# Kernel tuning notes

Hardware: AMD Instinct MI355X
Metric: run time of the kernel (lower is better)

## Reference

```python
import jax, jax.numpy as jnp
import numpy as np

EXP, MAN = 8, 23  # exponent/mantissa bits of the simulated float format


def float_quantize(x, exp=EXP, man=MAN):
    """Round-to-nearest-even quantization to a float format with `exp` exponent
    bits and `man` mantissa bits (faithful to mptorch float_quantize 'nearest').
    With exp=8, man=23 this is an exact identity on fp32 inputs."""
    emax = 2 ** (exp - 1) - 1          # max unbiased exponent
    emin = 1 - emax                     # min normal exponent (clamping here yields subnormal grid)
    ax = jnp.abs(x)
    e = jnp.clip(jnp.floor(jnp.log2(jnp.where(ax > 0, ax, 1.0))), emin, emax)
    # scale mantissa into [1,2), round to `man` fractional bits (ties-to-even via jnp.round)
    m = jnp.round(x * jnp.exp2(-e) * (2.0 ** man)) * (2.0 ** -man)
    q = m * jnp.exp2(e)
    maxval = (2.0 - 2.0 ** -man) * (2.0 ** emax)
    q = jnp.clip(q, -maxval, maxval)
    return jnp.where(ax == 0, x, q).astype(x.dtype)


def setup_inputs() -> dict:
    key = jax.random.key(0)
    k1, k2, k3 = jax.random.split(key, 3)
    M, IN, OUT = 8192, 1024, 4096
    x = jax.random.normal(k1, (M, IN), dtype=jnp.float32)
    # kaiming-uniform-ish scale for weight, 1/sqrt(fan_in) for bias
    bound_w = float(np.sqrt(1.0 / IN))
    weight = jax.random.uniform(k2, (OUT, IN), dtype=jnp.float32, minval=-bound_w, maxval=bound_w)
    bias = jax.random.uniform(k3, (OUT,), dtype=jnp.float32, minval=-bound_w, maxval=bound_w)
    return {"x": x, "weight": weight, "bias": bias}


def reference(x, weight, bias):
    # QLinearFunction.forward: quantize weight, quant_gemm, add quantized bias, quantize output.
    # quant_gemm with (man=23, exp=8) simulates fp32 multiply-accumulate, i.e. a plain
    # fp32 GEMM; we express it as matmul followed by output quantization.
    qweight = float_quantize(weight)                 # [OUT, IN]
    out = jnp.matmul(x, qweight.T)                   # [M, OUT], fp32 accumulate
    out = out + float_quantize(bias)[None, :]
    return float_quantize(out)
```

## Files before the change

kernel.cpp:

```cpp
#include <hip/hip_runtime.h>
#include <stdint.h>

#define MM 8192
#define KK 1024
#define NN 4096

#define BM 128
#define BN 128
#define BK 64

using f32x4 = __attribute__((ext_vector_type(4))) float;
using u16x8 = __attribute__((ext_vector_type(8))) unsigned short;

static __device__ __forceinline__ unsigned short f2bf(float f) {
    unsigned int u = __builtin_bit_cast(unsigned int, f);
    u += 0x7fffu + ((u >> 16) & 1u);
    return (unsigned short)(u >> 16);
}
static __device__ __forceinline__ float bf2f(unsigned short s) {
    unsigned int u = ((unsigned int)s) << 16;
    return __builtin_bit_cast(float, u);
}

__global__ __launch_bounds__(256) void split_hi_lo(const float* __restrict__ in,
                                                   unsigned short* __restrict__ hi,
                                                   unsigned short* __restrict__ lo,
                                                   int n8) {
    int i = blockIdx.x * 256 + threadIdx.x;
    if (i >= n8) return;
    const float4* p = (const float4*)in + (size_t)i * 2;
    float4 a = p[0], b = p[1];
    float v[8] = {a.x, a.y, a.z, a.w, b.x, b.y, b.z, b.w};
    u16x8 h, l;
#pragma unroll
    for (int j = 0; j < 8; ++j) {
        unsigned short hb = f2bf(v[j]);
        h[j] = hb;
        l[j] = f2bf(v[j] - bf2f(hb));
    }
    *((u16x8*)hi + i) = h;
    *((u16x8*)lo + i) = l;
}

static __device__ __forceinline__ void mfma16(f32x4& d, u16x8 a, u16x8 b) {
    asm("v_mfma_f32_16x16x32_bf16 %0, %1, %2, %0" : "+v"(d) : "v"(a), "v"(b));
}

__global__ __launch_bounds__(256, 2) void qlinear_mfma(
        const unsigned short* __restrict__ Ah, const unsigned short* __restrict__ Al,
        const unsigned short* __restrict__ Bh, const unsigned short* __restrict__ Bl,
        const float* __restrict__ bias, float* __restrict__ out) {
    __shared__ __attribute__((aligned(16))) unsigned short sAh[BM * BK];
    __shared__ __attribute__((aligned(16))) unsigned short sAl[BM * BK];
    __shared__ __attribute__((aligned(16))) unsigned short sBh[BN * BK];
    __shared__ __attribute__((aligned(16))) unsigned short sBl[BN * BK];

    int bid = blockIdx.x;
    int wg = (bid & 7) * 256 + (bid >> 3);
    int bm = wg & 63;
    int bn = wg >> 6;

    const int t = threadIdx.x;
    const int lane = t & 63;
    const int wid = t >> 6;

    const int wr = (wid >> 1) * 64;
    const int wc = (wid & 1) * 64;
    const int lr = lane & 15;
    const int lg = lane >> 4;

    f32x4 acc[4][4] = {};

    for (int kt = 0; kt < KK; kt += BK) {
        __syncthreads();
#pragma unroll
        for (int i = 0; i < 4; ++i) {
            int o = i * 256 + t;
            int row = o >> 3;
            int k0 = (o & 7) * 8;
            int sidx = row * BK + (k0 ^ ((row & 7) << 3));
            size_t ga = (size_t)(bm * BM + row) * KK + kt + k0;
            size_t gb = (size_t)(bn * BN + row) * KK + kt + k0;
            *(u16x8*)(sAh + sidx) = *(const u16x8*)(Ah + ga);
            *(u16x8*)(sAl + sidx) = *(const u16x8*)(Al + ga);
            *(u16x8*)(sBh + sidx) = *(const u16x8*)(Bh + gb);
            *(u16x8*)(sBl + sidx) = *(const u16x8*)(Bl + gb);
        }
        __syncthreads();

#pragma unroll
        for (int kk = 0; kk < 2; ++kk) {
            const int kb = kk * 32 + lg * 8;
            u16x8 ah[4], al[4], bh[4], bl[4];
#pragma unroll
            for (int mi = 0; mi < 4; ++mi) {
                int row = wr + mi * 16 + lr;
                int idx = row * BK + (kb ^ ((row & 7) << 3));
                ah[mi] = *(const u16x8*)(sAh + idx);
                al[mi] = *(const u16x8*)(sAl + idx);
            }
#pragma unroll
            for (int ni = 0; ni < 4; ++ni) {
                int row = wc + ni * 16 + lr;
                int idx = row * BK + (kb ^ ((row & 7) << 3));
                bh[ni] = *(const u16x8*)(sBh + idx);
                bl[ni] = *(const u16x8*)(sBl + idx);
            }
#pragma unroll
            for (int mi = 0; mi < 4; ++mi) {
#pragma unroll
                for (int ni = 0; ni < 4; ++ni) {
                    mfma16(acc[mi][ni], ah[mi], bh[ni]);
                    mfma16(acc[mi][ni], al[mi], bh[ni]);
                    mfma16(acc[mi][ni], ah[mi], bl[ni]);
                }
            }
        }
    }

    const int colbase = bn * BN + wc;
    const int rowbase = bm * BM + wr;
    float bv[4];
#pragma unroll
    for (int ni = 0; ni < 4; ++ni) bv[ni] = bias[colbase + ni * 16 + lr];
#pragma unroll
    for (int mi = 0; mi < 4; ++mi) {
#pragma unroll
        for (int ni = 0; ni < 4; ++ni) {
            int col = colbase + ni * 16 + lr;
            size_t base = (size_t)(rowbase + mi * 16 + lg * 4) * NN + col;
#pragma unroll
            for (int r = 0; r < 4; ++r)
                out[base + (size_t)r * NN] = acc[mi][ni][r] + bv[ni];
        }
    }
}

__global__ __launch_bounds__(256) void qlinear_naive(const float* __restrict__ x,
                                                     const float* __restrict__ w,
                                                     const float* __restrict__ bias,
                                                     float* __restrict__ out) {
    int n = blockIdx.x * 64 + (threadIdx.x & 63);
    int m = blockIdx.y * 4 + (threadIdx.x >> 6);
    const float4* xr = (const float4*)(x + (size_t)m * KK);
    const float4* wr = (const float4*)(w + (size_t)n * KK);
    float s = 0.f;
    for (int k = 0; k < KK / 4; ++k) {
        float4 a = xr[k], b = wr[k];
        s += a.x * b.x + a.y * b.y + a.z * b.z + a.w * b.w;
    }
    out[(size_t)m * NN + n] = s + bias[n];
}

extern "C" void kernel_launch(void* const* d_in, const int* in_sizes, int n_in,
                              void* d_out, int out_size, void* d_ws, size_t ws_size,
                              hipStream_t stream) {
    (void)in_sizes; (void)n_in; (void)out_size;
    const float* x = (const float*)d_in[0];
    const float* w = (const float*)d_in[1];
    const float* bias = (const float*)d_in[2];
    float* out = (float*)d_out;

    const size_t xcnt = (size_t)MM * KK;
    const size_t wcnt = (size_t)NN * KK;
    const size_t need = (xcnt + wcnt) * 2 * sizeof(unsigned short);

    if (ws_size >= need) {
        unsigned short* xh = (unsigned short*)d_ws;
        unsigned short* xl = xh + xcnt;
        unsigned short* wh = xl + xcnt;
        unsigned short* wl = wh + wcnt;
        split_hi_lo<<<(int)(xcnt / 8 / 256), 256, 0, stream>>>(x, xh, xl, (int)(xcnt / 8));
        split_hi_lo<<<(int)(wcnt / 8 / 256), 256, 0, stream>>>(w, wh, wl, (int)(wcnt / 8));
        qlinear_mfma<<<2048, 256, 0, stream>>>(xh, xl, wh, wl, bias, out);
    } else {
        dim3 grid(NN / 64, MM / 4);
        qlinear_naive<<<grid, 256, 0, stream>>>(x, w, bias, out);
    }
}
```

Measured before the change: 347.8 us.

## Pre-pack tiles and double-buffer 256x256 MFMA GEMM with direct global-to-LDS loads

The split kernel now writes the bf16 hi/lo operands in a pre-tiled, pre-swizzled layout, so every K-tile is one contiguous block. The GEMM switches to 256x256 tiles with 512 threads and a double-buffered LDS. It fills the next buffer with global_load_lds while MFMAs run, interleaving LDS reads, barriers and priority hints in phases. The goal is to hide global-load latency and raise per-block data reuse, at the cost of larger register and LDS use and fewer blocks (512).

```diff
diff --git a/kernel.cpp b/kernel.cpp
--- a/kernel.cpp
+++ b/kernel.cpp
@@ -4,13 +4,13 @@
 #define MM 8192
 #define KK 1024
 #define NN 4096
-
-#define BM 128
-#define BN 128
-#define BK 64
-
-using f32x4 = __attribute__((ext_vector_type(4))) float;
-using u16x8 = __attribute__((ext_vector_type(8))) unsigned short;
+#define NT 32
+#define TE 8192
+#define PL 16384
+
+typedef float f32x4 __attribute__((ext_vector_type(4)));
+typedef __bf16 bf16x8 __attribute__((ext_vector_type(8)));
+typedef unsigned short u16x8 __attribute__((ext_vector_type(8)));
 
 static __device__ __forceinline__ unsigned short f2bf(float f) {
     unsigned int u = __builtin_bit_cast(unsigned int, f);
@@ -22,14 +22,16 @@
     return __builtin_bit_cast(float, u);
 }
 
-__global__ __launch_bounds__(256) void split_hi_lo(const float* __restrict__ in,
-                                                   unsigned short* __restrict__ hi,
-                                                   unsigned short* __restrict__ lo,
-                                                   int n8) {
+__global__ __launch_bounds__(256) void split_pack(const float* __restrict__ in,
+        unsigned short* __restrict__ hi, unsigned short* __restrict__ lo, int total) {
     int i = blockIdx.x * 256 + threadIdx.x;
-    if (i >= n8) return;
-    const float4* p = (const float4*)in + (size_t)i * 2;
-    float4 a = p[0], b = p[1];
+    if (i >= total) return;
+    int row = i >> 7;
+    int og  = i & 127;
+    int kt  = og >> 2, oct = og & 3;
+    int bt  = row >> 8, r = row & 255;
+    const float4* s = (const float4*)(in + (size_t)row * KK + kt * 32 + oct * 8);
+    float4 a = s[0], b = s[1];
     float v[8] = {a.x, a.y, a.z, a.w, b.x, b.y, b.z, b.w};
     u16x8 h, l;
 #pragma unroll
@@ -38,102 +40,150 @@
         h[j] = hb;
         l[j] = f2bf(v[j] - bf2f(hb));
     }
-    *((u16x8*)hi + i) = h;
-    *((u16x8*)lo + i) = l;
-}
-
-static __device__ __forceinline__ void mfma16(f32x4& d, u16x8 a, u16x8 b) {
-    asm("v_mfma_f32_16x16x32_bf16 %0, %1, %2, %0" : "+v"(d) : "v"(a), "v"(b));
-}
-
-__global__ __launch_bounds__(256, 2) void qlinear_mfma(
+    int slot = r * 4 + (oct ^ ((r >> 1) & 3));
+    size_t off = (size_t)(bt * NT + kt) * TE + (size_t)slot * 8;
+    *(u16x8*)(hi + off) = h;
+    *(u16x8*)(lo + off) = l;
+}
+
+static __device__ __forceinline__ bf16x8 ldsr(unsigned addr) {
+    bf16x8 r;
+    asm volatile("ds_read_b128 %0, %1" : "=v"(r) : "v"(addr));
+    return r;
+}
+static __device__ __forceinline__ void gl16(const unsigned short* g, unsigned short* l) {
+    __builtin_amdgcn_global_load_lds(
+        (__attribute__((address_space(1))) void*)(void*)g,
+        (__attribute__((address_space(3))) void*)(void*)l, 16, 0, 0);
+}
+static __device__ __forceinline__ void mf(f32x4& d, bf16x8 a, bf16x8 b) {
+    d = __builtin_amdgcn_mfma_f32_16x16x32_bf16(a, b, d, 0, 0, 0);
+}
+
+#define PHASE_PRE() \
+    __builtin_amdgcn_s_barrier(); \
+    asm volatile("s_waitcnt lgkmcnt(0)" ::: "memory"); \
+    __builtin_amdgcn_sched_barrier(0); \
+    __builtin_amdgcn_s_setprio(1);
+#define PHASE_POST() \
+    __builtin_amdgcn_s_setprio(0); \
+    __builtin_amdgcn_s_barrier();
+#define CLUSTER(M0, M1) \
+    _Pragma("unroll") \
+    for (int ni = 0; ni < 4; ++ni) { \
+        mf(acc[M0][ni], a0, bh[ni]); mf(acc[M0][ni], l0, bh[ni]); mf(acc[M0][ni], a0, blo[ni]); \
+        mf(acc[M1][ni], a1, bh[ni]); mf(acc[M1][ni], l1, bh[ni]); mf(acc[M1][ni], a1, blo[ni]); \
+    }
+
+__global__ __launch_bounds__(512, 2) void qlinear_mfma(
         const unsigned short* __restrict__ Ah, const unsigned short* __restrict__ Al,
         const unsigned short* __restrict__ Bh, const unsigned short* __restrict__ Bl,
         const float* __restrict__ bias, float* __restrict__ out) {
-    __shared__ __attribute__((aligned(16))) unsigned short sAh[BM * BK];
-    __shared__ __attribute__((aligned(16))) unsigned short sAl[BM * BK];
-    __shared__ __attribute__((aligned(16))) unsigned short sBh[BN * BK];
-    __shared__ __attribute__((aligned(16))) unsigned short sBl[BN * BK];
+    __shared__ __attribute__((aligned(16))) unsigned short S[2][4][TE];
 
     int bid = blockIdx.x;
-    int wg = (bid & 7) * 256 + (bid >> 3);
-    int bm = wg & 63;
-    int bn = wg >> 6;
-
-    const int t = threadIdx.x;
-    const int lane = t & 63;
-    const int wid = t >> 6;
-
-    const int wr = (wid >> 1) * 64;
-    const int wc = (wid & 1) * 64;
-    const int lr = lane & 15;
-    const int lg = lane >> 4;
-
-    f32x4 acc[4][4] = {};
-
-    for (int kt = 0; kt < KK; kt += BK) {
-        __syncthreads();
-#pragma unroll
-        for (int i = 0; i < 4; ++i) {
-            int o = i * 256 + t;
-            int row = o >> 3;
-            int k0 = (o & 7) * 8;
-            int sidx = row * BK + (k0 ^ ((row & 7) << 3));
-            size_t ga = (size_t)(bm * BM + row) * KK + kt + k0;
-            size_t gb = (size_t)(bn * BN + row) * KK + kt + k0;
-            *(u16x8*)(sAh + sidx) = *(const u16x8*)(Ah + ga);
-            *(u16x8*)(sAl + sidx) = *(const u16x8*)(Al + ga);
-            *(u16x8*)(sBh + sidx) = *(const u16x8*)(Bh + gb);
-            *(u16x8*)(sBl + sidx) = *(const u16x8*)(Bl + gb);
-        }
-        __syncthreads();
-
-#pragma unroll
-        for (int kk = 0; kk < 2; ++kk) {
-            const int kb = kk * 32 + lg * 8;
-            u16x8 ah[4], al[4], bh[4], bl[4];
-#pragma unroll
-            for (int mi = 0; mi < 4; ++mi) {
-                int row = wr + mi * 16 + lr;
-                int idx = row * BK + (kb ^ ((row & 7) << 3));
-                ah[mi] = *(const u16x8*)(sAh + idx);
-                al[mi] = *(const u16x8*)(sAl + idx);
-            }
-#pragma unroll
-            for (int ni = 0; ni < 4; ++ni) {
-                int row = wc + ni * 16 + lr;
-                int idx = row * BK + (kb ^ ((row & 7) << 3));
-                bh[ni] = *(const u16x8*)(sBh + idx);
-                bl[ni] = *(const u16x8*)(sBl + idx);
-            }
-#pragma unroll
-            for (int mi = 0; mi < 4; ++mi) {
-#pragma unroll
-                for (int ni = 0; ni < 4; ++ni) {
-                    mfma16(acc[mi][ni], ah[mi], bh[ni]);
-                    mfma16(acc[mi][ni], al[mi], bh[ni]);
-                    mfma16(acc[mi][ni], ah[mi], bl[ni]);
-                }
-            }
-        }
-    }
-
-    const int colbase = bn * BN + wc;
-    const int rowbase = bm * BM + wr;
+    int wg = (bid & 7) * 64 + (bid >> 3);
+    int bm = wg & 31, bn = wg >> 5;
+
+    const int tix = threadIdx.x;
+    const int lane = tix & 63, wid = tix >> 6;
+    const int wr = (wid >> 2) * 128, wc = (wid & 3) * 64;
+    const int lr = lane & 15, lg = lane >> 4;
+    const int xorv = (lr >> 1) & 3;
+
+    const unsigned lb = (unsigned)(uintptr_t)(__attribute__((address_space(3))) void*)&S[0][0][0];
+    const unsigned pA = lb + (unsigned)(((wr + lr) * 32 + (lg ^ xorv) * 8) * 2);
+    const unsigned pB = lb + (unsigned)(((wc + lr) * 32 + (lg ^ xorv) * 8) * 2);
+
+    const int soff = wid * 1024 + lane * 8;
+    const unsigned short* sAh = Ah + (size_t)bm * NT * TE + soff;
+    const unsigned short* sAl = Al + (size_t)bm * NT * TE + soff;
+    const unsigned short* sBh = Bh + (size_t)bn * NT * TE + soff;
+    const unsigned short* sBl = Bl + (size_t)bn * NT * TE + soff;
+
+    f32x4 acc[8][4];
+#pragma unroll
+    for (int mi = 0; mi < 8; ++mi)
+#pragma unroll
+        for (int ni = 0; ni < 4; ++ni) acc[mi][ni] = (f32x4){0.f, 0.f, 0.f, 0.f};
+
+    gl16(sAh,       &S[0][0][wid * 1024]);
+    gl16(sAh + 512, &S[0][0][wid * 1024 + 512]);
+    gl16(sAl,       &S[0][1][wid * 1024]);
+    gl16(sAl + 512, &S[0][1][wid * 1024 + 512]);
+    gl16(sBh,       &S[0][2][wid * 1024]);
+    gl16(sBh + 512, &S[0][2][wid * 1024 + 512]);
+    gl16(sBl,       &S[0][3][wid * 1024]);
+    gl16(sBl + 512, &S[0][3][wid * 1024 + 512]);
+    asm volatile("s_waitcnt vmcnt(0)" ::: "memory");
+    __builtin_amdgcn_s_barrier();
+
+    for (int t = 0; t < NT; ++t) {
+        const unsigned bo = (unsigned)(t & 1) * (4 * PL);
+        const int nb = (t & 1) ^ 1;
+        const size_t st = (size_t)(t + 1) * TE;
+        const bool pf = (t + 1 < NT);
+
+        bf16x8 bh[4], blo[4], a0, a1, l0, l1;
+
+#pragma unroll
+        for (int ni = 0; ni < 4; ++ni) {
+            bh[ni]  = ldsr(pB + bo + 2 * PL + ni * 1024);
+            blo[ni] = ldsr(pB + bo + 3 * PL + ni * 1024);
+        }
+        a0 = ldsr(pA + bo);        l0 = ldsr(pA + bo + PL);
+        a1 = ldsr(pA + bo + 1024); l1 = ldsr(pA + bo + PL + 1024);
+        if (pf) {
+            gl16(sAh + st,       &S[nb][0][wid * 1024]);
+            gl16(sAh + st + 512, &S[nb][0][wid * 1024 + 512]);
+            gl16(sAl + st,       &S[nb][1][wid * 1024]);
+            gl16(sAl + st + 512, &S[nb][1][wid * 1024 + 512]);
+        }
+        PHASE_PRE();
+        CLUSTER(0, 1);
+        PHASE_POST();
+
+        a0 = ldsr(pA + bo + 2 * 1024); l0 = ldsr(pA + bo + PL + 2 * 1024);
+        a1 = ldsr(pA + bo + 3 * 1024); l1 = ldsr(pA + bo + PL + 3 * 1024);
+        if (pf) {
+            gl16(sBh + st,       &S[nb][2][wid * 1024]);
+            gl16(sBh + st + 512, &S[nb][2][wid * 1024 + 512]);
+            gl16(sBl + st,       &S[nb][3][wid * 1024]);
+            gl16(sBl + st + 512, &S[nb][3][wid * 1024 + 512]);
+        }
+        PHASE_PRE();
+        CLUSTER(2, 3);
+        PHASE_POST();
+
+        a0 = ldsr(pA + bo + 4 * 1024); l0 = ldsr(pA + bo + PL + 4 * 1024);
+        a1 = ldsr(pA + bo + 5 * 1024); l1 = ldsr(pA + bo + PL + 5 * 1024);
+        PHASE_PRE();
+        CLUSTER(4, 5);
+        PHASE_POST();
+
+        a0 = ldsr(pA + bo + 6 * 1024); l0 = ldsr(pA + bo + PL + 6 * 1024);
+        a1 = ldsr(pA + bo + 7 * 1024); l1 = ldsr(pA + bo + PL + 7 * 1024);
+        PHASE_PRE();
+        CLUSTER(6, 7);
+        __builtin_amdgcn_s_setprio(0);
+        asm volatile("s_waitcnt vmcnt(0)" ::: "memory");
+        __builtin_amdgcn_s_barrier();
+    }
+
+    const int row0 = bm * 256 + wr + lg * 4;
+    const int col0 = bn * 256 + wc + lr;
     float bv[4];
 #pragma unroll
-    for (int ni = 0; ni < 4; ++ni) bv[ni] = bias[colbase + ni * 16 + lr];
-#pragma unroll
-    for (int mi = 0; mi < 4; ++mi) {
+    for (int ni = 0; ni < 4; ++ni) bv[ni] = bias[col0 + ni * 16];
+#pragma unroll
+    for (int mi = 0; mi < 8; ++mi)
 #pragma unroll
         for (int ni = 0; ni < 4; ++ni) {
-            int col = colbase + ni * 16 + lr;
-            size_t base = (size_t)(rowbase + mi * 16 + lg * 4) * NN + col;
+            float* o = out + (size_t)(row0 + mi * 16) * NN + col0 + ni * 16;
 #pragma unroll
             for (int r = 0; r < 4; ++r)
-                out[base + (size_t)r * NN] = acc[mi][ni][r] + bv[ni];
-        }
-    }
+                o[(size_t)r * NN] = acc[mi][ni][r] + bv[ni];
+        }
 }
 
 __global__ __launch_bounds__(256) void qlinear_naive(const float* __restrict__ x,
@@ -170,9 +220,9 @@
         unsigned short* xl = xh + xcnt;
         unsigned short* wh = xl + xcnt;
         unsigned short* wl = wh + wcnt;
-        split_hi_lo<<<(int)(xcnt / 8 / 256), 256, 0, stream>>>(x, xh, xl, (int)(xcnt / 8));
-        split_hi_lo<<<(int)(wcnt / 8 / 256), 256, 0, stream>>>(w, wh, wl, (int)(wcnt / 8));
-        qlinear_mfma<<<2048, 256, 0, stream>>>(xh, xl, wh, wl, bias, out);
+        split_pack<<<(int)(MM * 128 / 256), 256, 0, stream>>>(x, xh, xl, MM * 128);
+        split_pack<<<(int)(NN * 128 / 256), 256, 0, stream>>>(w, wh, wl, NN * 128);
+        qlinear_mfma<<<512, 512, 0, stream>>>(xh, xl, wh, wl, bias, out);
     } else {
         dim3 grid(NN / 64, MM / 4);
         qlinear_naive<<<grid, 256, 0, stream>>>(x, w, bias, out);
```

Measured after the change: 335.3 us. -3.6%, faster.

## Pre-pack operands into MFMA fragment layout and use 32x32 MFMA with direct register A loads

Applied to the files above, without the earlier changes.

The split kernels now write bf16 hi/lo data in a tile-major fragment order. The A operand is loaded straight from global memory into registers, and the B operand is streamed into double-buffered LDS with global_load_lds. The GEMM changes to 256x128 tiles using 32x32x16 bf16 MFMA, with software prefetch of the next k-step and setprio around MFMA blocks. The aim is to remove LDS staging and bank traffic for A, cut LDS read instructions, and overlap loads with compute. In exchange it uses more registers, and A reuse across warps relies on L2/cache rather than shared memory.

```diff
diff --git a/kernel.cpp b/kernel.cpp
--- a/kernel.cpp
+++ b/kernel.cpp
@@ -4,13 +4,11 @@
 #define MM 8192
 #define KK 1024
 #define NN 4096
-
-#define BM 128
-#define BN 128
-#define BK 64
-
-using f32x4 = __attribute__((ext_vector_type(4))) float;
-using u16x8 = __attribute__((ext_vector_type(8))) unsigned short;
+#define NT 32
+
+typedef float f32x16 __attribute__((ext_vector_type(16)));
+typedef __bf16 bf16x8 __attribute__((ext_vector_type(8)));
+typedef unsigned short u16x8 __attribute__((ext_vector_type(8)));
 
 static __device__ __forceinline__ unsigned short f2bf(float f) {
     unsigned int u = __builtin_bit_cast(unsigned int, f);
@@ -22,14 +20,14 @@
     return __builtin_bit_cast(float, u);
 }
 
-__global__ __launch_bounds__(256) void split_hi_lo(const float* __restrict__ in,
-                                                   unsigned short* __restrict__ hi,
-                                                   unsigned short* __restrict__ lo,
-                                                   int n8) {
+__global__ __launch_bounds__(256) void pack_a(const float* __restrict__ x,
+        unsigned short* __restrict__ Ah, unsigned short* __restrict__ Al) {
     int i = blockIdx.x * 256 + threadIdx.x;
-    if (i >= n8) return;
-    const float4* p = (const float4*)in + (size_t)i * 2;
-    float4 a = p[0], b = p[1];
+    int lane = i & 63, fb = (i >> 6) & 15, kt = (i >> 10) & 31, bm = i >> 15;
+    int row = bm * 256 + (fb >> 1) * 32 + (lane & 31);
+    int k   = kt * 32 + (fb & 1) * 16 + (lane >> 5) * 8;
+    const float4* s = (const float4*)(x + (size_t)row * KK + k);
+    float4 a = s[0], b = s[1];
     float v[8] = {a.x, a.y, a.z, a.w, b.x, b.y, b.z, b.w};
     u16x8 h, l;
 #pragma unroll
@@ -38,102 +36,153 @@
         h[j] = hb;
         l[j] = f2bf(v[j] - bf2f(hb));
     }
-    *((u16x8*)hi + i) = h;
-    *((u16x8*)lo + i) = l;
-}
-
-static __device__ __forceinline__ void mfma16(f32x4& d, u16x8 a, u16x8 b) {
-    asm("v_mfma_f32_16x16x32_bf16 %0, %1, %2, %0" : "+v"(d) : "v"(a), "v"(b));
+    *(u16x8*)(Ah + (size_t)i * 8) = h;
+    *(u16x8*)(Al + (size_t)i * 8) = l;
+}
+
+__global__ __launch_bounds__(256) void pack_b(const float* __restrict__ w,
+        unsigned short* __restrict__ Bpk) {
+    int i = blockIdx.x * 256 + threadIdx.x;
+    int lane = i & 63, fb = (i >> 6) & 7, kt = (i >> 9) & 31, bn = i >> 14;
+    int col = bn * 128 + (fb >> 1) * 32 + (lane & 31);
+    int k   = kt * 32 + (fb & 1) * 16 + (lane >> 5) * 8;
+    const float4* s = (const float4*)(w + (size_t)col * KK + k);
+    float4 a = s[0], b = s[1];
+    float v[8] = {a.x, a.y, a.z, a.w, b.x, b.y, b.z, b.w};
+    u16x8 h, l;
+#pragma unroll
+    for (int j = 0; j < 8; ++j) {
+        unsigned short hb = f2bf(v[j]);
+        h[j] = hb;
+        l[j] = f2bf(v[j] - bf2f(hb));
+    }
+    size_t tb = ((size_t)bn * 32 + kt) * 8192;
+    *(u16x8*)(Bpk + tb + fb * 512 + lane * 8) = h;
+    *(u16x8*)(Bpk + tb + 4096 + fb * 512 + lane * 8) = l;
+}
+
+static __device__ __forceinline__ void gl16(const unsigned short* g, unsigned short* l) {
+    __builtin_amdgcn_global_load_lds(
+        (__attribute__((address_space(1))) void*)(void*)g,
+        (__attribute__((address_space(3))) void*)(void*)l, 16, 0, 0);
+}
+static __device__ __forceinline__ void mf(f32x16& d, bf16x8 a, bf16x8 b) {
+    d = __builtin_amdgcn_mfma_f32_32x32x16_bf16(a, b, d, 0, 0, 0);
 }
 
 __global__ __launch_bounds__(256, 2) void qlinear_mfma(
         const unsigned short* __restrict__ Ah, const unsigned short* __restrict__ Al,
-        const unsigned short* __restrict__ Bh, const unsigned short* __restrict__ Bl,
+        const unsigned short* __restrict__ Bpk,
         const float* __restrict__ bias, float* __restrict__ out) {
-    __shared__ __attribute__((aligned(16))) unsigned short sAh[BM * BK];
-    __shared__ __attribute__((aligned(16))) unsigned short sAl[BM * BK];
-    __shared__ __attribute__((aligned(16))) unsigned short sBh[BN * BK];
-    __shared__ __attribute__((aligned(16))) unsigned short sBl[BN * BK];
+    __shared__ __attribute__((aligned(16))) unsigned short sB[2 * 8192];
 
     int bid = blockIdx.x;
-    int wg = (bid & 7) * 256 + (bid >> 3);
-    int bm = wg & 63;
-    int bn = wg >> 6;
-
-    const int t = threadIdx.x;
-    const int lane = t & 63;
-    const int wid = t >> 6;
-
-    const int wr = (wid >> 1) * 64;
-    const int wc = (wid & 1) * 64;
-    const int lr = lane & 15;
-    const int lg = lane >> 4;
-
-    f32x4 acc[4][4] = {};
-
-    for (int kt = 0; kt < KK; kt += BK) {
+    int xc = bid & 7, s = bid >> 3;
+    int bm = (xc & 3) * 8 + (s & 7);
+    int bn = (xc >> 2) * 16 + (s >> 3);
+
+    const int tid = threadIdx.x;
+    const int lane = tid & 63, wid = tid >> 6;
+    const int wrb = (wid >> 1) * 4;
+    const int wcb = (wid & 1) * 2;
+
+    const size_t aoff = (size_t)bm * 262144 + (size_t)wrb * 1024 + lane * 8;
+    const size_t bsrc = (size_t)bn * 262144 + tid * 8;
+    const unsigned boff = wcb * 1024 + lane * 8;
+
+    f32x16 acc[4][2];
+#pragma unroll
+    for (int mi = 0; mi < 4; ++mi)
+#pragma unroll
+        for (int ni = 0; ni < 2; ++ni)
+#pragma unroll
+            for (int r = 0; r < 16; ++r) acc[mi][ni][r] = 0.f;
+
+    bf16x8 A0h[4], A0l[4], A1h[4], A1l[4];
+
+#define LDA(H, L, T, KS) do { _Pragma("unroll") \
+    for (int mi = 0; mi < 4; ++mi) { \
+        H[mi] = *(const bf16x8*)(Ah + aoff + (size_t)(T) * 8192 + mi * 1024 + (KS) * 512); \
+        L[mi] = *(const bf16x8*)(Al + aoff + (size_t)(T) * 8192 + mi * 1024 + (KS) * 512); \
+    } } while (0)
+#define STB(T, NB) do { _Pragma("unroll") \
+    for (int j = 0; j < 4; ++j) \
+        gl16(Bpk + bsrc + (size_t)(T) * 8192 + j * 2048, \
+             sB + (NB) * 8192 + j * 2048 + tid * 8); } while (0)
+
+    LDA(A0h, A0l, 0, 0);
+    LDA(A1h, A1l, 0, 1);
+    STB(0, 0);
+    __syncthreads();
+
+    for (int t = 0; t < NT; ++t) {
+        const int cur = t & 1, nb = cur ^ 1;
+        const unsigned short* sb = sB + cur * 8192;
+
+        bf16x8 B0h[2], B0l[2], B1h[2], B1l[2];
+#pragma unroll
+        for (int ni = 0; ni < 2; ++ni) {
+            B0h[ni] = *(const bf16x8*)(sb + boff + ni * 1024);
+            B0l[ni] = *(const bf16x8*)(sb + 4096 + boff + ni * 1024);
+        }
+        if (t + 1 < NT) STB(t + 1, nb);
+
+        __builtin_amdgcn_s_setprio(1);
+#pragma unroll
+        for (int mi = 0; mi < 4; ++mi)
+#pragma unroll
+            for (int ni = 0; ni < 2; ++ni) mf(acc[mi][ni], A0h[mi], B0h[ni]);
+#pragma unroll
+        for (int mi = 0; mi < 4; ++mi)
+#pragma unroll
+            for (int ni = 0; ni < 2; ++ni) mf(acc[mi][ni], A0l[mi], B0h[ni]);
+#pragma unroll
+        for (int mi = 0; mi < 4; ++mi)
+#pragma unroll
+            for (int ni = 0; ni < 2; ++ni) mf(acc[mi][ni], A0h[mi], B0l[ni]);
+        __builtin_amdgcn_s_setprio(0);
+        __builtin_amdgcn_sched_barrier(0);
+        if (t + 1 < NT) LDA(A0h, A0l, t + 1, 0);
+
+#pragma unroll
+        for (int ni = 0; ni < 2; ++ni) {
+            B1h[ni] = *(const bf16x8*)(sb + boff + ni * 1024 + 512);
+            B1l[ni] = *(const bf16x8*)(sb + 4096 + boff + ni * 1024 + 512);
+        }
+        __builtin_amdgcn_s_setprio(1);
+#pragma unroll
+        for (int mi = 0; mi < 4; ++mi)
+#pragma unroll
+            for (int ni = 0; ni < 2; ++ni) mf(acc[mi][ni], A1h[mi], B1h[ni]);
+#pragma unroll
+        for (int mi = 0; mi < 4; ++mi)
+#pragma unroll
+            for (int ni = 0; ni < 2; ++ni) mf(acc[mi][ni], A1l[mi], B1h[ni]);
+#pragma unroll
+        for (int mi = 0; mi < 4; ++mi)
+#pragma unroll
+            for (int ni = 0; ni < 2; ++ni) mf(acc[mi][ni], A1h[mi], B1l[ni]);
+        __builtin_amdgcn_s_setprio(0);
+        __builtin_amdgcn_sched_barrier(0);
+        if (t + 1 < NT) LDA(A1h, A1l, t + 1, 1);
+
         __syncthreads();
-#pragma unroll
-        for (int i = 0; i < 4; ++i) {
-            int o = i * 256 + t;
-            int row = o >> 3;
-            int k0 = (o & 7) * 8;
-            int sidx = row * BK + (k0 ^ ((row & 7) << 3));
-            size_t ga = (size_t)(bm * BM + row) * KK + kt + k0;
-            size_t gb = (size_t)(bn * BN + row) * KK + kt + k0;
-            *(u16x8*)(sAh + sidx) = *(const u16x8*)(Ah + ga);
-            *(u16x8*)(sAl + sidx) = *(const u16x8*)(Al + ga);
-            *(u16x8*)(sBh + sidx) = *(const u16x8*)(Bh + gb);
-            *(u16x8*)(sBl + sidx) = *(const u16x8*)(Bl + gb);
-        }
-        __syncthreads();
-
-#pragma unroll
-        for (int kk = 0; kk < 2; ++kk) {
-            const int kb = kk * 32 + lg * 8;
-            u16x8 ah[4], al[4], bh[4], bl[4];
-#pragma unroll
-            for (int mi = 0; mi < 4; ++mi) {
-                int row = wr + mi * 16 + lr;
-                int idx = row * BK + (kb ^ ((row & 7) << 3));
-                ah[mi] = *(const u16x8*)(sAh + idx);
-                al[mi] = *(const u16x8*)(sAl + idx);
+    }
+#undef LDA
+#undef STB
+
+    const int row0 = bm * 256 + (wid >> 1) * 128 + 4 * (lane >> 5);
+    const int col0 = bn * 128 + (wid & 1) * 64 + (lane & 31);
+    float bv[2] = {bias[col0], bias[col0 + 32]};
+#pragma unroll
+    for (int mi = 0; mi < 4; ++mi)
+#pragma unroll
+        for (int ni = 0; ni < 2; ++ni)
+#pragma unroll
+            for (int r = 0; r < 16; ++r) {
+                int rr = row0 + mi * 32 + (r & 3) + 8 * (r >> 2);
+                out[(size_t)rr * NN + col0 + ni * 32] = acc[mi][ni][r] + bv[ni];
             }
-#pragma unroll
-            for (int ni = 0; ni < 4; ++ni) {
-                int row = wc + ni * 16 + lr;
-                int idx = row * BK + (kb ^ ((row & 7) << 3));
-                bh[ni] = *(const u16x8*)(sBh + idx);
-                bl[ni] = *(const u16x8*)(sBl + idx);
-            }
-#pragma unroll
-            for (int mi = 0; mi < 4; ++mi) {
-#pragma unroll
-                for (int ni = 0; ni < 4; ++ni) {
-                    mfma16(acc[mi][ni], ah[mi], bh[ni]);
-                    mfma16(acc[mi][ni], al[mi], bh[ni]);
-                    mfma16(acc[mi][ni], ah[mi], bl[ni]);
-                }
-            }
-        }
-    }
-
-    const int colbase = bn * BN + wc;
-    const int rowbase = bm * BM + wr;
-    float bv[4];
-#pragma unroll
-    for (int ni = 0; ni < 4; ++ni) bv[ni] = bias[colbase + ni * 16 + lr];
-#pragma unroll
-    for (int mi = 0; mi < 4; ++mi) {
-#pragma unroll
-        for (int ni = 0; ni < 4; ++ni) {
-            int col = colbase + ni * 16 + lr;
-            size_t base = (size_t)(rowbase + mi * 16 + lg * 4) * NN + col;
-#pragma unroll
-            for (int r = 0; r < 4; ++r)
-                out[base + (size_t)r * NN] = acc[mi][ni][r] + bv[ni];
-        }
-    }
 }
 
 __global__ __launch_bounds__(256) void qlinear_naive(const float* __restrict__ x,
@@ -163,16 +212,15 @@
 
     const size_t xcnt = (size_t)MM * KK;
     const size_t wcnt = (size_t)NN * KK;
-    const size_t need = (xcnt + wcnt) * 2 * sizeof(unsigned short);
+    const size_t need = (2 * xcnt + 2 * wcnt) * sizeof(unsigned short);
 
     if (ws_size >= need) {
-        unsigned short* xh = (unsigned short*)d_ws;
-        unsigned short* xl = xh + xcnt;
-        unsigned short* wh = xl + xcnt;
-        unsigned short* wl = wh + wcnt;
-        split_hi_lo<<<(int)(xcnt / 8 / 256), 256, 0, stream>>>(x, xh, xl, (int)(xcnt / 8));
-        split_hi_lo<<<(int)(wcnt / 8 / 256), 256, 0, stream>>>(w, wh, wl, (int)(wcnt / 8));
-        qlinear_mfma<<<2048, 256, 0, stream>>>(xh, xl, wh, wl, bias, out);
+        unsigned short* Ahp = (unsigned short*)d_ws;
+        unsigned short* Alp = Ahp + xcnt;
+        unsigned short* Bp  = Alp + xcnt;
+        pack_a<<<(int)(xcnt / 8 / 256), 256, 0, stream>>>(x, Ahp, Alp);
+        pack_b<<<(int)(wcnt / 8 / 256), 256, 0, stream>>>(w, Bp);
+        qlinear_mfma<<<1024, 256, 0, stream>>>(Ahp, Alp, Bp, bias, out);
     } else {
         dim3 grid(NN / 64, MM / 4);
         qlinear_naive<<<grid, 256, 0, stream>>>(x, w, bias, out);
```

New measurement: 344.4 us. About the same (-1.0%).

## Pre-pack bf16 hi/lo planes into MFMA fragment order with 4-stage async LDS pipeline

Applied to the files above, without the earlier changes.

The pack kernels now write the bf16 hi/lo split of the inputs in a tiled layout that already matches the 32x32x16 MFMA fragment order. The GEMM loads tiles directly into LDS with global_load_lds, keeping three stages in flight across a four-buffer ring, and synchronises with explicit waitcnt and barrier calls. It also switches to 32x32x16 MFMA instructions, raises wave priority during the MFMA bursts, and remaps blocks into a grouped order for L2 reuse. The aim is to hide global memory latency and remove swizzle arithmetic and register-staged LDS stores. In exchange the code relies on hand-tuned waitcnt counts and a fixed layout, which makes it fragile.

```diff
diff --git a/kernel.cpp b/kernel.cpp
--- a/kernel.cpp
+++ b/kernel.cpp
@@ -4,13 +4,11 @@
 #define MM 8192
 #define KK 1024
 #define NN 4096
+#define NCH 64
 
-#define BM 128
-#define BN 128
-#define BK 64
-
-using f32x4 = __attribute__((ext_vector_type(4))) float;
-using u16x8 = __attribute__((ext_vector_type(8))) unsigned short;
+typedef float f32x16 __attribute__((ext_vector_type(16)));
+typedef __bf16 bf16x8 __attribute__((ext_vector_type(8)));
+typedef unsigned short u16x8 __attribute__((ext_vector_type(8)));
 
 static __device__ __forceinline__ unsigned short f2bf(float f) {
     unsigned int u = __builtin_bit_cast(unsigned int, f);
@@ -22,14 +20,15 @@
     return __builtin_bit_cast(float, u);
 }
 
-__global__ __launch_bounds__(256) void split_hi_lo(const float* __restrict__ in,
-                                                   unsigned short* __restrict__ hi,
-                                                   unsigned short* __restrict__ lo,
-                                                   int n8) {
+__global__ __launch_bounds__(256) void pack_planes(const float* __restrict__ in,
+        unsigned short* __restrict__ pk, int total) {
     int i = blockIdx.x * 256 + threadIdx.x;
-    if (i >= n8) return;
-    const float4* p = (const float4*)in + (size_t)i * 2;
-    float4 a = p[0], b = p[1];
+    if (i >= total) return;
+    int lane = i & 63, f = (i >> 6) & 3, kt = (i >> 8) & 63, bt = i >> 14;
+    int row = bt * 128 + f * 32 + (lane & 31);
+    int k   = kt * 16 + (lane >> 5) * 8;
+    const float4* s = (const float4*)(in + (size_t)row * KK + k);
+    float4 a = s[0], b = s[1];
     float v[8] = {a.x, a.y, a.z, a.w, b.x, b.y, b.z, b.w};
     u16x8 h, l;
 #pragma unroll
@@ -38,102 +37,115 @@
         h[j] = hb;
         l[j] = f2bf(v[j] - bf2f(hb));
     }
-    *((u16x8*)hi + i) = h;
-    *((u16x8*)lo + i) = l;
+    size_t tb = (size_t)(bt * 64 + kt) * 4096;
+    size_t fo = (size_t)f * 512 + lane * 8;
+    *(u16x8*)(pk + tb + fo) = h;
+    *(u16x8*)(pk + tb + 2048 + fo) = l;
 }
 
-static __device__ __forceinline__ void mfma16(f32x4& d, u16x8 a, u16x8 b) {
-    asm("v_mfma_f32_16x16x32_bf16 %0, %1, %2, %0" : "+v"(d) : "v"(a), "v"(b));
+static __device__ __forceinline__ bf16x8 ldsr(unsigned addr) {
+    bf16x8 r;
+    asm volatile("ds_read_b128 %0, %1" : "=v"(r) : "v"(addr));
+    return r;
+}
+static __device__ __forceinline__ void gl16(const unsigned short* g, unsigned short* l) {
+    __builtin_amdgcn_global_load_lds(
+        (__attribute__((address_space(1))) void*)(void*)g,
+        (__attribute__((address_space(3))) void*)(void*)l, 16, 0, 0);
+}
+static __device__ __forceinline__ void mf(f32x16& d, bf16x8 a, bf16x8 b) {
+    d = __builtin_amdgcn_mfma_f32_32x32x16_bf16(a, b, d, 0, 0, 0);
 }
 
 __global__ __launch_bounds__(256, 2) void qlinear_mfma(
-        const unsigned short* __restrict__ Ah, const unsigned short* __restrict__ Al,
-        const unsigned short* __restrict__ Bh, const unsigned short* __restrict__ Bl,
+        const unsigned short* __restrict__ Apk, const unsigned short* __restrict__ Bpk,
         const float* __restrict__ bias, float* __restrict__ out) {
-    __shared__ __attribute__((aligned(16))) unsigned short sAh[BM * BK];
-    __shared__ __attribute__((aligned(16))) unsigned short sAl[BM * BK];
-    __shared__ __attribute__((aligned(16))) unsigned short sBh[BN * BK];
-    __shared__ __attribute__((aligned(16))) unsigned short sBl[BN * BK];
+    __shared__ __attribute__((aligned(16))) unsigned short S[4][4][2048];
 
     int bid = blockIdx.x;
     int wg = (bid & 7) * 256 + (bid >> 3);
-    int bm = wg & 63;
-    int bn = wg >> 6;
+    int c = wg >> 8, sub = wg & 255;
+    int g = sub >> 4, r = sub & 15;
+    int bm = (c & 3) * 16 + (g >> 2) * 4 + (r >> 2);
+    int bn = (c >> 2) * 16 + (g & 3) * 4 + (r & 3);
 
-    const int t = threadIdx.x;
-    const int lane = t & 63;
-    const int wid = t >> 6;
+    const int tid = threadIdx.x;
+    const int lane = tid & 63, wid = tid >> 6;
+    const int wr = wid >> 1, wc = wid & 1;
 
-    const int wr = (wid >> 1) * 64;
-    const int wc = (wid & 1) * 64;
-    const int lr = lane & 15;
-    const int lg = lane >> 4;
+    const unsigned lb = (unsigned)(uintptr_t)(__attribute__((address_space(3))) void*)&S[0][0][0];
+    const unsigned aA = (unsigned)(wr * 2048 + lane * 16);
+    const unsigned aB = (unsigned)(8192 + wc * 2048 + lane * 16);
 
-    f32x4 acc[4][4] = {};
+    const size_t abase = (size_t)bm * 262144;
+    const size_t bbase = (size_t)bn * 262144;
 
-    for (int kt = 0; kt < KK; kt += BK) {
-        __syncthreads();
+#define STAGE(T) do {                                                        \
+        size_t ta = abase + (size_t)(T) * 4096, tb = bbase + (size_t)(T) * 4096; \
+        int bf = (T) & 3;                                                    \
+        gl16(Apk + ta + tid * 8,        &S[bf][0][tid * 8]);                 \
+        gl16(Apk + ta + 2048 + tid * 8, &S[bf][1][tid * 8]);                 \
+        gl16(Bpk + tb + tid * 8,        &S[bf][2][tid * 8]);                 \
+        gl16(Bpk + tb + 2048 + tid * 8, &S[bf][3][tid * 8]);                 \
+    } while (0)
+
+    f32x16 acc[2][2];
 #pragma unroll
-        for (int i = 0; i < 4; ++i) {
-            int o = i * 256 + t;
-            int row = o >> 3;
-            int k0 = (o & 7) * 8;
-            int sidx = row * BK + (k0 ^ ((row & 7) << 3));
-            size_t ga = (size_t)(bm * BM + row) * KK + kt + k0;
-            size_t gb = (size_t)(bn * BN + row) * KK + kt + k0;
-            *(u16x8*)(sAh + sidx) = *(const u16x8*)(Ah + ga);
-            *(u16x8*)(sAl + sidx) = *(const u16x8*)(Al + ga);
-            *(u16x8*)(sBh + sidx) = *(const u16x8*)(Bh + gb);
-            *(u16x8*)(sBl + sidx) = *(const u16x8*)(Bl + gb);
-        }
-        __syncthreads();
+    for (int mi = 0; mi < 2; ++mi)
+#pragma unroll
+        for (int ni = 0; ni < 2; ++ni)
+#pragma unroll
+            for (int q = 0; q < 16; ++q) acc[mi][ni][q] = 0.f;
 
+    STAGE(0); STAGE(1); STAGE(2);
+    asm volatile("s_waitcnt vmcnt(8)" ::: "memory");
+    __builtin_amdgcn_s_barrier();
+
+    for (int ct = 0; ct < NCH; ++ct) {
+        const unsigned cb = lb + (unsigned)(ct & 3) * 16384u;
+        bf16x8 Ah0 = ldsr(cb + aA);
+        bf16x8 Ah1 = ldsr(cb + aA + 1024u);
+        bf16x8 Bh0 = ldsr(cb + aB);
+        bf16x8 Bh1 = ldsr(cb + aB + 1024u);
+        bf16x8 Al0 = ldsr(cb + aA + 4096u);
+        bf16x8 Al1 = ldsr(cb + aA + 5120u);
+        bf16x8 Bl0 = ldsr(cb + aB + 4096u);
+        bf16x8 Bl1 = ldsr(cb + aB + 5120u);
+        if (ct < NCH - 3) STAGE(ct + 3);
+
+        asm volatile("s_waitcnt lgkmcnt(4)" ::: "memory");
+        __builtin_amdgcn_sched_barrier(0);
+        __builtin_amdgcn_s_setprio(1);
+        mf(acc[0][0], Ah0, Bh0); mf(acc[0][1], Ah0, Bh1);
+        mf(acc[1][0], Ah1, Bh0); mf(acc[1][1], Ah1, Bh1);
+        asm volatile("s_waitcnt lgkmcnt(0)" ::: "memory");
+        __builtin_amdgcn_sched_barrier(0);
+        mf(acc[0][0], Al0, Bh0); mf(acc[0][1], Al0, Bh1);
+        mf(acc[1][0], Al1, Bh0); mf(acc[1][1], Al1, Bh1);
+        mf(acc[0][0], Ah0, Bl0); mf(acc[0][1], Ah0, Bl1);
+        mf(acc[1][0], Ah1, Bl0); mf(acc[1][1], Ah1, Bl1);
+        __builtin_amdgcn_s_setprio(0);
+        __builtin_amdgcn_sched_barrier(0);
+
+        if (ct <= NCH - 4)      { asm volatile("s_waitcnt vmcnt(8)" ::: "memory"); }
+        else if (ct == NCH - 3) { asm volatile("s_waitcnt vmcnt(4)" ::: "memory"); }
+        else if (ct == NCH - 2) { asm volatile("s_waitcnt vmcnt(0)" ::: "memory"); }
+        __builtin_amdgcn_s_barrier();
+    }
+#undef STAGE
+
+    const int row0 = bm * 128 + wr * 64 + 4 * (lane >> 5);
+    const int col0 = bn * 128 + wc * 64 + (lane & 31);
+    float bv[2] = {bias[col0], bias[col0 + 32]};
 #pragma unroll
-        for (int kk = 0; kk < 2; ++kk) {
-            const int kb = kk * 32 + lg * 8;
-            u16x8 ah[4], al[4], bh[4], bl[4];
+    for (int mi = 0; mi < 2; ++mi)
 #pragma unroll
-            for (int mi = 0; mi < 4; ++mi) {
-                int row = wr + mi * 16 + lr;
-                int idx = row * BK + (kb ^ ((row & 7) << 3));
-                ah[mi] = *(const u16x8*)(sAh + idx);
-                al[mi] = *(const u16x8*)(sAl + idx);
+        for (int ni = 0; ni < 2; ++ni)
+#pragma unroll
+            for (int q = 0; q < 16; ++q) {
+                int rr = row0 + mi * 32 + (q & 3) + 8 * (q >> 2);
+                out[(size_t)rr * NN + col0 + ni * 32] = acc[mi][ni][q] + bv[ni];
             }
-#pragma unroll
-            for (int ni = 0; ni < 4; ++ni) {
-                int row = wc + ni * 16 + lr;
-                int idx = row * BK + (kb ^ ((row & 7) << 3));
-                bh[ni] = *(const u16x8*)(sBh + idx);
-                bl[ni] = *(const u16x8*)(sBl + idx);
-            }
-#pragma unroll
-            for (int mi = 0; mi < 4; ++mi) {
-#pragma unroll
-                for (int ni = 0; ni < 4; ++ni) {
-                    mfma16(acc[mi][ni], ah[mi], bh[ni]);
-                    mfma16(acc[mi][ni], al[mi], bh[ni]);
-                    mfma16(acc[mi][ni], ah[mi], bl[ni]);
-                }
-            }
-        }
-    }
-
-    const int colbase = bn * BN + wc;
-    const int rowbase = bm * BM + wr;
-    float bv[4];
-#pragma unroll
-    for (int ni = 0; ni < 4; ++ni) bv[ni] = bias[colbase + ni * 16 + lr];
-#pragma unroll
-    for (int mi = 0; mi < 4; ++mi) {
-#pragma unroll
-        for (int ni = 0; ni < 4; ++ni) {
-            int col = colbase + ni * 16 + lr;
-            size_t base = (size_t)(rowbase + mi * 16 + lg * 4) * NN + col;
-#pragma unroll
-            for (int r = 0; r < 4; ++r)
-                out[base + (size_t)r * NN] = acc[mi][ni][r] + bv[ni];
-        }
-    }
 }
 
 __global__ __launch_bounds__(256) void qlinear_naive(const float* __restrict__ x,
@@ -163,16 +175,14 @@
 
     const size_t xcnt = (size_t)MM * KK;
     const size_t wcnt = (size_t)NN * KK;
-    const size_t need = (xcnt + wcnt) * 2 * sizeof(unsigned short);
+    const size_t need = (2 * xcnt + 2 * wcnt) * sizeof(unsigned short);
 
     if (ws_size >= need) {
-        unsigned short* xh = (unsigned short*)d_ws;
-        unsigned short* xl = xh + xcnt;
-        unsigned short* wh = xl + xcnt;
-        unsigned short* wl = wh + wcnt;
-        split_hi_lo<<<(int)(xcnt / 8 / 256), 256, 0, stream>>>(x, xh, xl, (int)(xcnt / 8));
-        split_hi_lo<<<(int)(wcnt / 8 / 256), 256, 0, stream>>>(w, wh, wl, (int)(wcnt / 8));
-        qlinear_mfma<<<2048, 256, 0, stream>>>(xh, xl, wh, wl, bias, out);
+        unsigned short* Apk = (unsigned short*)d_ws;
+        unsigned short* Bpk = Apk + 2 * xcnt;
+        pack_planes<<<(int)(xcnt / 8 / 256), 256, 0, stream>>>(x, Apk, (int)(xcnt / 8));
+        pack_planes<<<(int)(wcnt / 8 / 256), 256, 0, stream>>>(w, Bpk, (int)(wcnt / 8));
+        qlinear_mfma<<<2048, 256, 0, stream>>>(Apk, Bpk, bias, out);
     } else {
         dim3 grid(NN / 64, MM / 4);
         qlinear_naive<<<grid, 256, 0, stream>>>(x, w, bias, out);
```

Result: faster. 339.2 us (-2.5%).
